# Kernel tuning notes

Measured on AMD Instinct MI355X. Metric: run time of the kernel, lower is better.

## Reference

```python
import jax, jax.numpy as jnp
import numpy as np

NUM_NODES = 50000
NUM_EDGES = 800000
INPUT_DIM = 256
OUTPUT_DIM = 256
NUM_HEADS = 8
HEAD_DIM = OUTPUT_DIM // NUM_HEADS


def setup_inputs() -> dict:
    key = jax.random.key(0)
    ks = jax.random.split(key, 14)
    x = jax.random.normal(ks[0], (NUM_NODES, INPUT_DIM), dtype=jnp.float32)
    edge_index = jax.random.randint(ks[1], (2, NUM_EDGES), 0, NUM_NODES, dtype=jnp.int32)
    # timestamps in seconds over ~11.5 days so log1p(|dt|/3600) is informative
    edge_time = jax.random.uniform(ks[2], (NUM_EDGES,), dtype=jnp.float32) * 1e6
    node_time = jax.random.uniform(ks[3], (NUM_NODES,), dtype=jnp.float32) * 1e6
    s_in = 1.0 / np.sqrt(INPUT_DIM)
    s_out = 1.0 / np.sqrt(OUTPUT_DIM)
    s_t = 1.0 / np.sqrt(2.0)
    Wq = jax.random.uniform(ks[4], (INPUT_DIM, OUTPUT_DIM), jnp.float32, -s_in, s_in)
    bq = jax.random.uniform(ks[5], (OUTPUT_DIM,), jnp.float32, -s_in, s_in)
    Wk = jax.random.uniform(ks[6], (INPUT_DIM, OUTPUT_DIM), jnp.float32, -s_in, s_in)
    bk = jax.random.uniform(ks[7], (OUTPUT_DIM,), jnp.float32, -s_in, s_in)
    Wv = jax.random.uniform(ks[8], (INPUT_DIM, OUTPUT_DIM), jnp.float32, -s_in, s_in)
    bv = jax.random.uniform(ks[9], (OUTPUT_DIM,), jnp.float32, -s_in, s_in)
    Wt = jax.random.uniform(ks[10], (2, NUM_HEADS), jnp.float32, -s_t, s_t)
    bt = jax.random.uniform(ks[11], (NUM_HEADS,), jnp.float32, -s_t, s_t)
    Wo = jax.random.uniform(ks[12], (OUTPUT_DIM, OUTPUT_DIM), jnp.float32, -s_out, s_out)
    bo = jax.random.uniform(ks[13], (OUTPUT_DIM,), jnp.float32, -s_out, s_out)
    return {"x": x, "edge_index": edge_index, "edge_time": edge_time, "node_time": node_time,
            "Wq": Wq, "bq": bq, "Wk": Wk, "bk": bk, "Wv": Wv, "bv": bv,
            "Wt": Wt, "bt": bt, "Wo": Wo, "bo": bo}


def reference(x, edge_index, edge_time, node_time, Wq, bq, Wk, bk, Wv, bv, Wt, bt, Wo, bo):
    n = x.shape[0]
    q = (x @ Wq + bq).reshape(n, NUM_HEADS, HEAD_DIM)
    k = (x @ Wk + bk).reshape(n, NUM_HEADS, HEAD_DIM)
    v = (x @ Wv + bv).reshape(n, NUM_HEADS, HEAD_DIM)
    src, dst = edge_index[0], edge_index[1]
    # temporal features per edge
    time_diff = edge_time - node_time[dst]
    time_features = jnp.stack(
        [jnp.sign(time_diff), jnp.log1p(jnp.abs(time_diff) / 3600.0)], axis=-1)  # [E, 2]
    temporal_weights = time_features @ Wt + bt  # [E, H]
    scale = HEAD_DIM ** -0.5
    scores = jnp.einsum('ehd,ehd->eh', q[dst], k[src]) * scale + temporal_weights  # [E, H]
    # softmax over ALL edges per head (dim=0), as in the original
    alpha = jax.nn.softmax(scores, axis=0)  # [E, H]
    msg = alpha[..., None] * v[src]  # [E, H, D]
    out = jax.ops.segment_sum(msg, dst, num_segments=n)  # [N, H, D]
    out = out.reshape(n, OUTPUT_DIM)
    return out @ Wo + bo
```

## Files before the change

### kernel.cpp

```cpp
#include <hip/hip_runtime.h>
#include <hip/hip_bf16.h>

#define NUM_NODES 50000
#define NUM_EDGES 800000
#define NUM_HEADS 8
#define HEAD_DIM 32
#define SCAN_BLOCKS 49
#define NCHUNK32 1563

typedef unsigned short ushort8 __attribute__((ext_vector_type(8)));
typedef float f32x4 __attribute__((ext_vector_type(4)));
typedef __bf16 bf16x8 __attribute__((ext_vector_type(8)));
typedef _Float16 h2 __attribute__((ext_vector_type(2)));

union BF8 { ushort8 u; bf16x8 b; };
union H8 { ushort8 u; h2 h[4]; };

#if defined(__has_builtin)
#if __has_builtin(__builtin_amdgcn_fdot2)
#define FDOT2(a, b, c) __builtin_amdgcn_fdot2((a), (b), (c), false)
#endif
#endif
#ifndef FDOT2
#define FDOT2(a, b, c) ((float)(a)[0] * (float)(b)[0] + (float)(a)[1] * (float)(b)[1] + (c))
#endif

__device__ __forceinline__ unsigned float_to_key(float f) {
    int i = __float_as_int(f);
    return (i >= 0) ? ((unsigned)i | 0x80000000u) : ~(unsigned)i;
}
__device__ __forceinline__ float key_to_float(unsigned u) {
    unsigned b = (u & 0x80000000u) ? (u & 0x7fffffffu) : ~u;
    return __int_as_float((int)b);
}
__device__ __forceinline__ float bf2f(unsigned short u) {
    return __uint_as_float(((unsigned)u) << 16);
}
__device__ __forceinline__ unsigned short f2bf(float f) {
    unsigned u = __float_as_uint(f);
    unsigned r = (u + 0x7fffu + ((u >> 16) & 1u)) >> 16;
    return (unsigned short)r;
}
__device__ __forceinline__ unsigned short f2h(float f) {
    _Float16 h = (_Float16)f;
    return *(unsigned short*)&h;
}
__device__ __forceinline__ float h2f(unsigned short u) {
    _Float16 h = *(const _Float16*)&u;
    return (float)h;
}

__global__ __launch_bounds__(256) void deg_kernel(const int* __restrict__ dst_idx, int* __restrict__ deg) {
    int e = blockIdx.x * 256 + threadIdx.x;
    if (e < NUM_EDGES) atomicAdd(&deg[dst_idx[e]], 1);
}

__global__ __launch_bounds__(1024) void scanA_kernel(
    const int* __restrict__ deg, int* __restrict__ offs, int* __restrict__ blocksum)
{
    __shared__ int buf[1024];
    int tid = threadIdx.x;
    int i = blockIdx.x * 1024 + tid;
    int v = (i < NUM_NODES) ? deg[i] : 0;
    buf[tid] = v;
    __syncthreads();
    for (int off = 1; off < 1024; off <<= 1) {
        int t = (tid >= off) ? buf[tid - off] : 0;
        __syncthreads();
        buf[tid] += t;
        __syncthreads();
    }
    if (i < NUM_NODES) offs[i] = buf[tid] - v;
    if (tid == 1023) blocksum[blockIdx.x] = buf[1023];
}

__global__ __launch_bounds__(64) void scanB_kernel(
    const int* __restrict__ blocksum, int* __restrict__ carry, int* __restrict__ offs)
{
    if (threadIdx.x == 0) {
        int acc = 0;
        for (int b = 0; b < SCAN_BLOCKS; b++) { carry[b] = acc; acc += blocksum[b]; }
        offs[NUM_NODES] = acc;
    }
}

__global__ __launch_bounds__(256) void scanC_kernel(
    int* __restrict__ offs, const int* __restrict__ carry, int* __restrict__ cursor)
{
    int i = blockIdx.x * 256 + threadIdx.x;
    if (i < NUM_NODES) {
        int v = offs[i] + carry[i >> 10];
        offs[i] = v;
        cursor[i] = v;
    }
}

__global__ __launch_bounds__(256) void fillA_kernel(
    const int* __restrict__ dst_idx, int* __restrict__ cursor, int* __restrict__ edge_of)
{
    int e = blockIdx.x * 256 + threadIdx.x;
    if (e < NUM_EDGES) {
        int pos = atomicAdd(&cursor[dst_idx[e]], 1);
        edge_of[pos] = e;
    }
}

__global__ __launch_bounds__(256) void fillB_kernel(
    const int* __restrict__ edge_of,
    const int* __restrict__ src_idx, const int* __restrict__ dst_idx,
    const float* __restrict__ edge_time, const float* __restrict__ node_time,
    const float* __restrict__ Wt, const float* __restrict__ bt,
    unsigned* __restrict__ sdp, unsigned short* __restrict__ twh)
{
    int pos = blockIdx.x * 256 + threadIdx.x;
    if (pos < NUM_EDGES) {
        int e = __builtin_nontemporal_load(&edge_of[pos]);
        int s = src_idx[e];
        int d = dst_idx[e];
        __builtin_nontemporal_store((unsigned)s | ((unsigned)d << 16), &sdp[pos]);
        float td = edge_time[e] - node_time[d];
        float t0 = (td > 0.f) ? 1.f : ((td < 0.f) ? -1.f : 0.f);
        float t1 = log1pf(fabsf(td) * (1.f / 3600.f));
#pragma unroll
        for (int h = 0; h < 8; h++) {
            float tw = t0 * Wt[h] + t1 * Wt[8 + h] + bt[h];
            __builtin_nontemporal_store(f2h(tw), &twh[(size_t)h * NUM_EDGES + pos]);
        }
    }
}

__global__ __launch_bounds__(256) void wtrans_kernel(
    const float* __restrict__ Wq, const float* __restrict__ Wk,
    const float* __restrict__ Wv, const float* __restrict__ Wo,
    unsigned short* __restrict__ Wt)
{
    __shared__ float t[64][65];
    int nb = blockIdx.x * 64;
    int kb = blockIdx.y * 64;
    int g = nb >> 8;
    const float* W = (g == 0) ? Wq : (g == 1) ? Wk : (g == 2) ? Wv : Wo;
    int n0 = nb & 255;
    int tx = threadIdx.x & 63;
    int ty = threadIdx.x >> 6;
#pragma unroll
    for (int i = 0; i < 16; i++) {
        int k = i * 4 + ty;
        t[tx][k] = W[(size_t)(kb + k) * 256 + n0 + tx];
    }
    __syncthreads();
#pragma unroll
    for (int i = 0; i < 16; i++) {
        int n = i * 4 + ty;
        Wt[(size_t)(nb + n) * 256 + kb + tx] = f2bf(t[n][tx]);
    }
}

__global__ __launch_bounds__(256) void wpack_kernel(
    const unsigned short* __restrict__ Wt, unsigned short* __restrict__ Wpk)
{
    int gid = blockIdx.x * 256 + threadIdx.x;
    int lane = gid & 63;
    int fragidx = gid >> 6;
    int c2 = fragidx & 7;
    int nf = (fragidx >> 3) & 3;
    int cb = (fragidx >> 5) & 3;
    int g = fragidx >> 7;
    int l16 = lane & 15;
    int kg = lane >> 4;
    int n_col = g * 256 + cb * 64 + nf * 16 + l16;
    int k0 = c2 * 32 + kg * 8;
    ushort8 v = *(const ushort8*)(Wt + (size_t)n_col * 256 + k0);
    *(ushort8*)(Wpk + (size_t)gid * 8) = v;
}

__global__ __launch_bounds__(256) void gemm_qkv_mfma7(
    const float* __restrict__ A, int M,
    const unsigned short* __restrict__ Wpk,
    const float* __restrict__ b0, const float* __restrict__ b1, const float* __restrict__ b2,
    unsigned short* __restrict__ O0, unsigned short* __restrict__ O1, unsigned short* __restrict__ O2)
{
    __shared__ unsigned short As[64 * 256];
    int tid = threadIdx.x;
    int rowbase = blockIdx.x * 64;

    {
        int rsub = tid >> 6;
        int c4 = (tid & 63) * 4;
        int cchunk = (tid & 63) >> 1;
        int sub = (tid & 1);
#pragma unroll
        for (int it = 0; it < 16; it++) {
            int row = it * 4 + rsub;
            int grow = rowbase + row;
            float4 av = make_float4(0.f, 0.f, 0.f, 0.f);
            if (grow < M) av = *(const float4*)(A + (size_t)grow * 256 + c4);
            ushort4 o;
            o.x = f2bf(av.x); o.y = f2bf(av.y); o.z = f2bf(av.z); o.w = f2bf(av.w);
            unsigned byte = row * 512 + ((unsigned)(cchunk ^ (row & 7)) << 4) + sub * 8;
            *(ushort4*)((char*)As + byte) = o;
        }
    }
    __syncthreads();

    int lane = tid & 63;
    int wid = tid >> 6;
    int l16 = lane & 15;
    int kg = lane >> 4;

#pragma unroll
    for (int p = 0; p < 3; p++) {
        const float* bias = (p == 0) ? b0 : (p == 1) ? b1 : b2;
        unsigned short* O = (p == 0) ? O0 : (p == 1) ? O1 : O2;

        f32x4 acc[4][4];
#pragma unroll
        for (int m = 0; m < 4; m++)
#pragma unroll
            for (int n = 0; n < 4; n++) acc[m][n] = (f32x4)(0.0f);

        const ushort8* wbase = (const ushort8*)(Wpk + ((size_t)(p * 4 + wid) * 2048 + lane) * 8);

#pragma unroll
        for (int c2 = 0; c2 < 8; c2++) {
            bf16x8 wfr[4];
#pragma unroll
            for (int n = 0; n < 4; n++) {
                BF8 t; t.u = wbase[(n * 8 + c2) * 64];
                wfr[n] = t.b;
            }
            bf16x8 afr[4];
#pragma unroll
            for (int m = 0; m < 4; m++) {
                int row = m * 16 + l16;
                int cchunk = (c2 * 4 + kg) ^ (row & 7);
                BF8 t;
                t.u = *(const ushort8*)((const char*)As + row * 512 + (cchunk << 4));
                afr[m] = t.b;
            }
#pragma unroll
            for (int m = 0; m < 4; m++)
#pragma unroll
                for (int n = 0; n < 4; n++)
                    acc[m][n] = __builtin_amdgcn_mfma_f32_16x16x32_bf16(wfr[n], afr[m], acc[m][n], 0, 0, 0);
        }

#pragma unroll
        for (int m = 0; m < 4; m++) {
            int node = rowbase + m * 16 + l16;
            if (node >= M) continue;
#pragma unroll
            for (int n = 0; n < 4; n++) {
                int lc = wid * 64 + n * 16 + kg * 4;
                float4 bv = *(const float4*)(bias + lc);
                ushort4 o;
                if (p < 2) {
                    o.x = f2h(acc[m][n][0] + bv.x);
                    o.y = f2h(acc[m][n][1] + bv.y);
                    o.z = f2h(acc[m][n][2] + bv.z);
                    o.w = f2h(acc[m][n][3] + bv.w);
                } else {
                    o.x = f2bf(acc[m][n][0] + bv.x);
                    o.y = f2bf(acc[m][n][1] + bv.y);
                    o.z = f2bf(acc[m][n][2] + bv.z);
                    o.w = f2bf(acc[m][n][3] + bv.w);
                }
                int hh = lc >> 5, dd = lc & 31;
                *(ushort4*)(O + ((size_t)hh * NUM_NODES + node) * 32 + dd) = o;
            }
        }
    }
}

__global__ __launch_bounds__(256) void gemm_out_mfma6(
    const unsigned short* __restrict__ aggb, int M,
    const unsigned short* __restrict__ Wpk,
    const float* __restrict__ bias, const float* __restrict__ kscale,
    float* __restrict__ C)
{
    __shared__ unsigned short As[64 * 256];
    int tid = threadIdx.x;
    int rowbase = blockIdx.x * 64;

    {
        int rsub = tid >> 6;
        int c4 = (tid & 63) * 4;
        int cchunk = (tid & 63) >> 1;
        int sub = (tid & 1);
        int hh = c4 >> 5, dd = c4 & 31;
        float ks = kscale[hh];
#pragma unroll
        for (int it = 0; it < 16; it++) {
            int row = it * 4 + rsub;
            int grow = rowbase + row;
            ushort4 av = make_ushort4(0, 0, 0, 0);
            if (grow < M) av = *(const ushort4*)(aggb + ((size_t)hh * NUM_NODES + grow) * 32 + dd);
            ushort4 o;
            o.x = f2bf(bf2f(av.x) * ks); o.y = f2bf(bf2f(av.y) * ks);
            o.z = f2bf(bf2f(av.z) * ks); o.w = f2bf(bf2f(av.w) * ks);
            unsigned byte = row * 512 + ((unsigned)(cchunk ^ (row & 7)) << 4) + sub * 8;
            *(ushort4*)((char*)As + byte) = o;
        }
    }
    __syncthreads();

    int lane = tid & 63;
    int wid = tid >> 6;
    int l16 = lane & 15;
    int kg = lane >> 4;

    f32x4 acc[4][4];
#pragma unroll
    for (int m = 0; m < 4; m++)
#pragma unroll
        for (int n = 0; n < 4; n++) acc[m][n] = (f32x4)(0.0f);

    const ushort8* wbase = (const ushort8*)(Wpk + ((size_t)wid * 2048 + lane) * 8);

#pragma unroll
    for (int c2 = 0; c2 < 8; c2++) {
        bf16x8 wfr[4];
#pragma unroll
        for (int n = 0; n < 4; n++) {
            BF8 t; t.u = wbase[(n * 8 + c2) * 64];
            wfr[n] = t.b;
        }
        bf16x8 afr[4];
#pragma unroll
        for (int m = 0; m < 4; m++) {
            int row = m * 16 + l16;
            int cchunk = (c2 * 4 + kg) ^ (row & 7);
            BF8 t;
            t.u = *(const ushort8*)((const char*)As + row * 512 + (cchunk << 4));
            afr[m] = t.b;
        }
#pragma unroll
        for (int m = 0; m < 4; m++)
#pragma unroll
            for (int n = 0; n < 4; n++)
                acc[m][n] = __builtin_amdgcn_mfma_f32_16x16x32_bf16(wfr[n], afr[m], acc[m][n], 0, 0, 0);
    }

#pragma unroll
    for (int m = 0; m < 4; m++) {
        int node = rowbase + m * 16 + l16;
        if (node >= M) continue;
#pragma unroll
        for (int n = 0; n < 4; n++) {
            int col = wid * 64 + n * 16 + kg * 4;
            float4 bv = *(const float4*)(bias + col);
            float4 o;
            o.x = acc[m][n][0] + bv.x;
            o.y = acc[m][n][1] + bv.y;
            o.z = acc[m][n][2] + bv.z;
            o.w = acc[m][n][3] + bv.w;
            *(float4*)(C + (size_t)node * 256 + col) = o;
        }
    }
}

__global__ __launch_bounds__(256) void score6_kernel(
    const unsigned short* __restrict__ qh, const unsigned short* __restrict__ kh,
    const unsigned* __restrict__ sdp, const unsigned short* __restrict__ twh,
    unsigned short* __restrict__ scores, unsigned* __restrict__ partialmax)
{
    __shared__ unsigned sm;
    int tid = threadIdx.x;
    if (tid == 0) sm = 0u;
    __syncthreads();
    int h = blockIdx.x & 7;
    int blk = blockIdx.x >> 3;
    const unsigned short* qhh = qh + (size_t)h * NUM_NODES * 32;
    const unsigned short* khh = kh + (size_t)h * NUM_NODES * 32;
    const unsigned short* tw_h = twh + (size_t)h * NUM_EDGES;
    unsigned short* sc_h = scores + (size_t)h * NUM_EDGES;
    unsigned mykey = 0u;
    const int stride = 256 * 256;
    for (int pos = blk * 256 + tid; pos < NUM_EDGES; pos += stride) {
        unsigned sdv = __builtin_nontemporal_load(&sdp[pos]);
        int s = sdv & 0xffffu;
        int d = sdv >> 16;
        float tw = h2f(__builtin_nontemporal_load(&tw_h[pos]));
        const ushort8* qp = (const ushort8*)(qhh + (size_t)d * 32);
        const ushort8* kp = (const ushort8*)(khh + (size_t)s * 32);
        float dotv = 0.f;
#pragma unroll
        for (int i = 0; i < 4; i++) {
            H8 a, b;
            a.u = qp[i]; b.u = kp[i];
#pragma unroll
            for (int j = 0; j < 4; j++) dotv = FDOT2(a.h[j], b.h[j], dotv);
        }
        float sc = dotv * 0.17677669529663687f + tw;
        __builtin_nontemporal_store(f2h(sc), &sc_h[pos]);
        unsigned kkey = float_to_key(sc);
        mykey = (kkey > mykey) ? kkey : mykey;
    }
#pragma unroll
    for (int off = 32; off > 0; off >>= 1) {
        unsigned o = __shfl_xor(mykey, off, 64);
        mykey = (o > mykey) ? o : mykey;
    }
    if ((tid & 63) == 0) atomicMax(&sm, mykey);
    __syncthreads();
    if (tid == 0) partialmax[blockIdx.x] = sm;
}

__global__ __launch_bounds__(256) void reduce_max3_kernel(
    const unsigned* __restrict__ partialmax, float* __restrict__ headmax)
{
    int tid = threadIdx.x;
    int h = tid >> 5, lane = tid & 31;
    unsigned m = 0u;
    for (int i = lane; i < 256; i += 32) {
        unsigned v = partialmax[i * 8 + h];
        m = (v > m) ? v : m;
    }
    for (int off = 16; off > 0; off >>= 1) {
        unsigned o = __shfl_down(m, off, 32);
        m = (o > m) ? o : m;
    }
    if (lane == 0) headmax[h] = key_to_float(m);
}

__global__ __launch_bounds__(256) void aggregate9_kernel(
    const unsigned short* __restrict__ vh, const unsigned short* __restrict__ scores,
    const unsigned* __restrict__ sdp, const int* __restrict__ offs,
    const float* __restrict__ headmax, unsigned short* __restrict__ aggb,
    float* __restrict__ psum_part)
{
    __shared__ int sSrc[512];
    __shared__ float sP[512];
    __shared__ float blocksum;
    int tid = threadIdx.x;
    int h = blockIdx.x & 7;
    int chunk = blockIdx.x >> 3;
    int nodebase = chunk * 32;
    int g = tid >> 3;
    int ln = tid & 7;
    int node = nodebase + g;
    float m = headmax[h];
    const unsigned short* sc_h = scores + (size_t)h * NUM_EDGES;
    const unsigned short* vhh = vh + (size_t)h * NUM_NODES * 32;
    if (tid == 0) blocksum = 0.f;

    int blkstart = offs[nodebase];
    int blkend = offs[(nodebase + 32 < NUM_NODES) ? (nodebase + 32) : NUM_NODES];
    int start = 0, end = 0;
    if (node < NUM_NODES) { start = offs[node]; end = offs[node + 1]; }

    f32x4 a0 = (f32x4)(0.f), a1 = (f32x4)(0.f);
    float ps = 0.f;

    for (int t0 = blkstart; t0 < blkend; t0 += 512) {
        int cnt = min(512, blkend - t0);
        __syncthreads();
        for (int i = tid; i < cnt; i += 256) {
            sSrc[i] = (int)(__builtin_nontemporal_load(&sdp[t0 + i]) & 0xffffu);
            float p = __expf(h2f(__builtin_nontemporal_load(&sc_h[t0 + i])) - m);
            sP[i] = p;
            ps += p;
        }
        __syncthreads();
        int lo = (start > t0) ? start : t0;
        int hi = (end < t0 + cnt) ? end : (t0 + cnt);
        int cb = lo;
        for (; cb + 2 <= hi; cb += 2) {
            int i0 = cb - t0;
            int s0 = sSrc[i0], s1 = sSrc[i0 + 1];
            float p0 = sP[i0], p1 = sP[i0 + 1];
            ushort4 v0 = *(const ushort4*)(vhh + (size_t)s0 * 32 + ln * 4);
            ushort4 v1 = *(const ushort4*)(vhh + (size_t)s1 * 32 + ln * 4);
            a0[0] += p0 * bf2f(v0.x); a0[1] += p0 * bf2f(v0.y);
            a0[2] += p0 * bf2f(v0.z); a0[3] += p0 * bf2f(v0.w);
            a1[0] += p1 * bf2f(v1.x); a1[1] += p1 * bf2f(v1.y);
            a1[2] += p1 * bf2f(v1.z); a1[3] += p1 * bf2f(v1.w);
        }
        if (cb < hi) {
            int i0 = cb - t0;
            int s0 = sSrc[i0];
            float p0 = sP[i0];
            ushort4 v0 = *(const ushort4*)(vhh + (size_t)s0 * 32 + ln * 4);
            a0[0] += p0 * bf2f(v0.x); a0[1] += p0 * bf2f(v0.y);
            a0[2] += p0 * bf2f(v0.z); a0[3] += p0 * bf2f(v0.w);
        }
    }

    if (node < NUM_NODES) {
        ushort4 o;
        o.x = f2bf(a0[0] + a1[0]); o.y = f2bf(a0[1] + a1[1]);
        o.z = f2bf(a0[2] + a1[2]); o.w = f2bf(a0[3] + a1[3]);
        *(ushort4*)(aggb + ((size_t)h * NUM_NODES + node) * 32 + ln * 4) = o;
    }

    __syncthreads();
#pragma unroll
    for (int off = 32; off > 0; off >>= 1) ps += __shfl_xor(ps, off, 64);
    if ((tid & 63) == 0) atomicAdd(&blocksum, ps);
    __syncthreads();
    if (tid == 0) psum_part[blockIdx.x] = blocksum;
}

__global__ __launch_bounds__(256) void reduce_psum2_kernel(
    const float* __restrict__ psum_part, float* __restrict__ headinv)
{
    int tid = threadIdx.x;
    int h = tid >> 5, lane = tid & 31;
    float s = 0.f;
    for (int i = lane; i < NCHUNK32; i += 32) s += psum_part[i * 8 + h];
    for (int off = 16; off > 0; off >>= 1) s += __shfl_down(s, off, 32);
    if (lane == 0) headinv[h] = 1.f / s;
}

extern "C" void kernel_launch(void* const* d_in, const int* in_sizes, int n_in,
                              void* d_out, int out_size, void* d_ws, size_t ws_size,
                              hipStream_t stream) {
    const float* x = (const float*)d_in[0];
    const int* ei = (const int*)d_in[1];
    const int* src_idx = ei;
    const int* dst_idx = ei + NUM_EDGES;
    const float* edge_time = (const float*)d_in[2];
    const float* node_time = (const float*)d_in[3];
    const float* Wq = (const float*)d_in[4];  const float* bq = (const float*)d_in[5];
    const float* Wk = (const float*)d_in[6];  const float* bk = (const float*)d_in[7];
    const float* Wv = (const float*)d_in[8];  const float* bv = (const float*)d_in[9];
    const float* Wt = (const float*)d_in[10]; const float* bt = (const float*)d_in[11];
    const float* Wo = (const float*)d_in[12]; const float* bo = (const float*)d_in[13];
    float* out = (float*)d_out;

    char* w = (char*)d_ws;
    unsigned short* qb = (unsigned short*)w; w += (size_t)NUM_NODES * 256 * 2;
    unsigned short* kb = (unsigned short*)w; w += (size_t)NUM_NODES * 256 * 2;
    unsigned short* vb = (unsigned short*)w; w += (size_t)NUM_NODES * 256 * 2;
    unsigned short* scores = (unsigned short*)w; w += (size_t)NUM_EDGES * 8 * 2;
    unsigned short* twh = (unsigned short*)w; w += (size_t)NUM_EDGES * 8 * 2;
    unsigned short* aggb = (unsigned short*)w; w += (size_t)NUM_NODES * 256 * 2;
    unsigned* sdp = (unsigned*)w;   w += (size_t)NUM_EDGES * 4;
    int* edge_of = (int*)w;         w += (size_t)NUM_EDGES * 4;
    int* deg = (int*)w;             w += (size_t)NUM_NODES * 4;
    int* offs = (int*)w;            w += (size_t)(NUM_NODES + 1) * 4;
    int* cursor = (int*)w;          w += (size_t)NUM_NODES * 4;
    unsigned* partialmax = (unsigned*)w; w += 2048 * 4;
    float* psum_part = (float*)w;   w += (size_t)NCHUNK32 * 8 * 4;
    float* headmax = (float*)w;     w += 8 * 4;
    float* headinv = (float*)w;     w += 8 * 4;
    int* blocksum = (int*)w;        w += 64 * 4;
    int* bcarry = (int*)w;          w += 64 * 4;
    unsigned short* Wtb = (unsigned short*)w; w += (size_t)1024 * 256 * 2;
    unsigned short* Wpk = (unsigned short*)w; w += (size_t)1024 * 256 * 2;

    hipMemsetAsync(deg, 0, (size_t)NUM_NODES * 4, stream);

    dim3 gw(16, 4);
    wtrans_kernel<<<gw, 256, 0, stream>>>(Wq, Wk, Wv, Wo, Wtb);
    wpack_kernel<<<128, 256, 0, stream>>>(Wtb, Wpk);

    deg_kernel<<<(NUM_EDGES + 255) / 256, 256, 0, stream>>>(dst_idx, deg);
    scanA_kernel<<<SCAN_BLOCKS, 1024, 0, stream>>>(deg, offs, blocksum);
    scanB_kernel<<<1, 64, 0, stream>>>(blocksum, bcarry, offs);
    scanC_kernel<<<(NUM_NODES + 255) / 256, 256, 0, stream>>>(offs, bcarry, cursor);
    fillA_kernel<<<(NUM_EDGES + 255) / 256, 256, 0, stream>>>(dst_idx, cursor, edge_of);
    fillB_kernel<<<(NUM_EDGES + 255) / 256, 256, 0, stream>>>(
        edge_of, src_idx, dst_idx, edge_time, node_time, Wt, bt, sdp, twh);

    gemm_qkv_mfma7<<<(NUM_NODES + 63) / 64, 256, 0, stream>>>(
        x, NUM_NODES, Wpk, bq, bk, bv, qb, kb, vb);

    score6_kernel<<<2048, 256, 0, stream>>>(qb, kb, sdp, twh, scores, partialmax);
    reduce_max3_kernel<<<1, 256, 0, stream>>>(partialmax, headmax);

    aggregate9_kernel<<<NCHUNK32 * 8, 256, 0, stream>>>(
        vb, scores, sdp, offs, headmax, aggb, psum_part);
    reduce_psum2_kernel<<<1, 256, 0, stream>>>(psum_part, headinv);

    gemm_out_mfma6<<<(NUM_NODES + 63) / 64, 256, 0, stream>>>(
        aggb, NUM_NODES, Wpk + (size_t)768 * 256, bo, headinv, out);
}
```

Baseline: 382.9 us.

## Store per-edge time features instead of per-head weights; quad-split score dot

fillB now writes only the two temporal features per edge, packed as halves, instead of eight per-head temporal weights. score computes the Wt/bt projection inline, which cuts the edge-sized buffer traffic. The score kernel also splits each 32-element q·k dot across four lanes that each do one 16-byte load and reduce with shuffles, for more memory parallelism per edge. The aggregate kernel switches sdp/score loads from nontemporal to normal loads so they can hit cache. Rounding the features to half precision before the projection changes numerics slightly.

```diff
diff --git a/kernel.cpp b/kernel.cpp
--- a/kernel.cpp
+++ b/kernel.cpp
@@ -109,8 +109,7 @@
     const int* __restrict__ edge_of,
     const int* __restrict__ src_idx, const int* __restrict__ dst_idx,
     const float* __restrict__ edge_time, const float* __restrict__ node_time,
-    const float* __restrict__ Wt, const float* __restrict__ bt,
-    unsigned* __restrict__ sdp, unsigned short* __restrict__ twh)
+    unsigned* __restrict__ sdp, unsigned* __restrict__ tfh)
 {
     int pos = blockIdx.x * 256 + threadIdx.x;
     if (pos < NUM_EDGES) {
@@ -121,11 +120,7 @@
         float td = edge_time[e] - node_time[d];
         float t0 = (td > 0.f) ? 1.f : ((td < 0.f) ? -1.f : 0.f);
         float t1 = log1pf(fabsf(td) * (1.f / 3600.f));
-#pragma unroll
-        for (int h = 0; h < 8; h++) {
-            float tw = t0 * Wt[h] + t1 * Wt[8 + h] + bt[h];
-            __builtin_nontemporal_store(f2h(tw), &twh[(size_t)h * NUM_EDGES + pos]);
-        }
+        __builtin_nontemporal_store((unsigned)f2h(t0) | ((unsigned)f2h(t1) << 16), &tfh[pos]);
     }
 }
 
@@ -358,9 +353,10 @@
     }
 }
 
-__global__ __launch_bounds__(256) void score6_kernel(
+__global__ __launch_bounds__(256) void score7_kernel(
     const unsigned short* __restrict__ qh, const unsigned short* __restrict__ kh,
-    const unsigned* __restrict__ sdp, const unsigned short* __restrict__ twh,
+    const unsigned* __restrict__ sdp, const unsigned* __restrict__ tfh,
+    const float* __restrict__ Wt, const float* __restrict__ bt,
     unsigned short* __restrict__ scores, unsigned* __restrict__ partialmax)
 {
     __shared__ unsigned sm;
@@ -369,29 +365,31 @@
     __syncthreads();
     int h = blockIdx.x & 7;
     int blk = blockIdx.x >> 3;
+    float wt0 = Wt[h], wt1 = Wt[8 + h], btv = bt[h];
     const unsigned short* qhh = qh + (size_t)h * NUM_NODES * 32;
     const unsigned short* khh = kh + (size_t)h * NUM_NODES * 32;
-    const unsigned short* tw_h = twh + (size_t)h * NUM_EDGES;
     unsigned short* sc_h = scores + (size_t)h * NUM_EDGES;
+    int quad = tid >> 2;
+    int lq = tid & 3;
     unsigned mykey = 0u;
-    const int stride = 256 * 256;
-    for (int pos = blk * 256 + tid; pos < NUM_EDGES; pos += stride) {
+    const int qstride = 256 * 64;
+    for (int pos = blk * 64 + quad; pos < NUM_EDGES; pos += qstride) {
         unsigned sdv = __builtin_nontemporal_load(&sdp[pos]);
+        unsigned tp = __builtin_nontemporal_load(&tfh[pos]);
         int s = sdv & 0xffffu;
         int d = sdv >> 16;
-        float tw = h2f(__builtin_nontemporal_load(&tw_h[pos]));
-        const ushort8* qp = (const ushort8*)(qhh + (size_t)d * 32);
-        const ushort8* kp = (const ushort8*)(khh + (size_t)s * 32);
+        H8 a, b;
+        a.u = *(const ushort8*)(qhh + (size_t)d * 32 + lq * 8);
+        b.u = *(const ushort8*)(khh + (size_t)s * 32 + lq * 8);
         float dotv = 0.f;
 #pragma unroll
-        for (int i = 0; i < 4; i++) {
-            H8 a, b;
-            a.u = qp[i]; b.u = kp[i];
-#pragma unroll
-            for (int j = 0; j < 4; j++) dotv = FDOT2(a.h[j], b.h[j], dotv);
-        }
-        float sc = dotv * 0.17677669529663687f + tw;
-        __builtin_nontemporal_store(f2h(sc), &sc_h[pos]);
+        for (int j = 0; j < 4; j++) dotv = FDOT2(a.h[j], b.h[j], dotv);
+        dotv += __shfl_xor(dotv, 1, 64);
+        dotv += __shfl_xor(dotv, 2, 64);
+        float t0 = h2f((unsigned short)(tp & 0xffffu));
+        float t1 = h2f((unsigned short)(tp >> 16));
+        float sc = dotv * 0.17677669529663687f + (t0 * wt0 + t1 * wt1 + btv);
+        if (lq == 0) __builtin_nontemporal_store(f2h(sc), &sc_h[pos]);
         unsigned kkey = float_to_key(sc);
         mykey = (kkey > mykey) ? kkey : mykey;
     }
@@ -422,7 +420,7 @@
     if (lane == 0) headmax[h] = key_to_float(m);
 }
 
-__global__ __launch_bounds__(256) void aggregate9_kernel(
+__global__ __launch_bounds__(256) void aggregate10_kernel(
     const unsigned short* __restrict__ vh, const unsigned short* __restrict__ scores,
     const unsigned* __restrict__ sdp, const int* __restrict__ offs,
     const float* __restrict__ headmax, unsigned short* __restrict__ aggb,
@@ -455,8 +453,8 @@
         int cnt = min(512, blkend - t0);
         __syncthreads();
         for (int i = tid; i < cnt; i += 256) {
-            sSrc[i] = (int)(__builtin_nontemporal_load(&sdp[t0 + i]) & 0xffffu);
-            float p = __expf(h2f(__builtin_nontemporal_load(&sc_h[t0 + i])) - m);
+            sSrc[i] = (int)(sdp[t0 + i] & 0xffffu);
+            float p = __expf(h2f(sc_h[t0 + i]) - m);
             sP[i] = p;
             ps += p;
         }
@@ -532,9 +530,9 @@
     unsigned short* kb = (unsigned short*)w; w += (size_t)NUM_NODES * 256 * 2;
     unsigned short* vb = (unsigned short*)w; w += (size_t)NUM_NODES * 256 * 2;
     unsigned short* scores = (unsigned short*)w; w += (size_t)NUM_EDGES * 8 * 2;
-    unsigned short* twh = (unsigned short*)w; w += (size_t)NUM_EDGES * 8 * 2;
     unsigned short* aggb = (unsigned short*)w; w += (size_t)NUM_NODES * 256 * 2;
     unsigned* sdp = (unsigned*)w;   w += (size_t)NUM_EDGES * 4;
+    unsigned* tfh = (unsigned*)w;   w += (size_t)NUM_EDGES * 4;
     int* edge_of = (int*)w;         w += (size_t)NUM_EDGES * 4;
     int* deg = (int*)w;             w += (size_t)NUM_NODES * 4;
     int* offs = (int*)w;            w += (size_t)(NUM_NODES + 1) * 4;
@@ -560,15 +558,15 @@
     scanC_kernel<<<(NUM_NODES + 255) / 256, 256, 0, stream>>>(offs, bcarry, cursor);
     fillA_kernel<<<(NUM_EDGES + 255) / 256, 256, 0, stream>>>(dst_idx, cursor, edge_of);
     fillB_kernel<<<(NUM_EDGES + 255) / 256, 256, 0, stream>>>(
-        edge_of, src_idx, dst_idx, edge_time, node_time, Wt, bt, sdp, twh);
+        edge_of, src_idx, dst_idx, edge_time, node_time, sdp, tfh);
 
     gemm_qkv_mfma7<<<(NUM_NODES + 63) / 64, 256, 0, stream>>>(
         x, NUM_NODES, Wpk, bq, bk, bv, qb, kb, vb);
 
-    score6_kernel<<<2048, 256, 0, stream>>>(qb, kb, sdp, twh, scores, partialmax);
+    score7_kernel<<<2048, 256, 0, stream>>>(qb, kb, sdp, tfh, Wt, bt, scores, partialmax);
     reduce_max3_kernel<<<1, 256, 0, stream>>>(partialmax, headmax);
 
-    aggregate9_kernel<<<NCHUNK32 * 8, 256, 0, stream>>>(
+    aggregate10_kernel<<<NCHUNK32 * 8, 256, 0, stream>>>(
         vb, scores, sdp, offs, headmax, aggb, psum_part);
     reduce_psum2_kernel<<<1, 256, 0, stream>>>(psum_part, headinv);
 
```

After: 382.1 us. Within noise of the previous version (-0.2%).
